# Kernel optimization log

Measured on AMD Instinct MI355X. Metric: run time of the kernel, lower is better.

## Reference

```python
import jax, jax.numpy as jnp
import numpy as np


def setup_inputs() -> dict:
    key = jax.random.key(0)
    k1, k2, k3 = jax.random.split(key, 3)
    B, H, S, D = 2, 16, 2048, 64
    q = jax.random.normal(k1, (B, H, S, D), dtype=jnp.float32)
    k = jax.random.normal(k2, (B, H, S, D), dtype=jnp.float32)
    v = jax.random.normal(k3, (B, H, S, D), dtype=jnp.float32)
    return {"q": q, "k": k, "v": v}


def reference(q, k, v):
    # q,k,v: [B,H,S,D]; causal attention with 1/sqrt(D) scaling, fp32 softmax.
    scale = 1.0 / (q.shape[-1] ** 0.5)
    scores = jnp.einsum('bhqd,bhkd->bhqk', q * scale, k)  # [B,H,S,S]
    S = scores.shape[-1]
    causal_mask = jnp.triu(jnp.ones((S, S), dtype=bool), k=1)
    scores = jnp.where(causal_mask, -jnp.inf, scores)
    attn = jax.nn.softmax(scores.astype(jnp.float32), axis=-1).astype(q.dtype)
    output = jnp.einsum('bhqk,bhkd->bhqd', attn, v)
    # Module also returns an all-zeros attn_weights placeholder of shape [B,H,S,S]
    attn_weights = jnp.zeros(scores.shape, dtype=q.dtype)
    return (output, attn_weights)
```

## Files before the change

kernel.cpp:

```cpp
#include <hip/hip_runtime.h>


typedef __bf16 bf16x8 __attribute__((ext_vector_type(8)));
typedef float f32x4 __attribute__((ext_vector_type(4)));

#define LOG2E 1.44269504088896340736f

__device__ __forceinline__ unsigned short f2bf(float f) {
  unsigned int u = __float_as_uint(f);
  u += 0x7fffu + ((u >> 16) & 1u);
  return (unsigned short)(u >> 16);
}

union U8 { unsigned short u[8]; bf16x8 v; };

constexpr int Sdim = 2048, Ddim = 64, BHn = 32;
constexpr int QTiles = Sdim / 64;
constexpr int LDK = 72;
constexpr int OUT0 = BHn * Sdim * Ddim;

__global__ __launch_bounds__(256, 2)
void flash_causal_kernel(const float* __restrict__ Q, const float* __restrict__ K,
                         const float* __restrict__ V, float* __restrict__ out) {
  __shared__ unsigned short Klds[64 * LDK];
  __shared__ unsigned short Vlds[Ddim * LDK];
  __shared__ unsigned short Plds[4][16 * LDK];

  const int tid  = threadIdx.x;
  const int wave = tid >> 6;
  const int lane = tid & 63;
  const int quad = lane >> 4;
  const int l15  = lane & 15;

  const int bh = blockIdx.x & (BHn - 1);
  const int g  = (int)(blockIdx.x >> 5);
  const int qt = (QTiles - 1) - g;

  const int base  = bh * Sdim * Ddim;
  const int qrow0 = qt * 64 + wave * 16;

  bf16x8 aq[2];
  {
    const float* qp = Q + base + (qrow0 + l15) * Ddim + quad * 8;
    #pragma unroll
    for (int s = 0; s < 2; ++s) {
      float4 a = *(const float4*)(qp + 32 * s);
      float4 b = *(const float4*)(qp + 32 * s + 4);
      U8 u;
      u.u[0] = f2bf(a.x * 0.125f); u.u[1] = f2bf(a.y * 0.125f);
      u.u[2] = f2bf(a.z * 0.125f); u.u[3] = f2bf(a.w * 0.125f);
      u.u[4] = f2bf(b.x * 0.125f); u.u[5] = f2bf(b.y * 0.125f);
      u.u[6] = f2bf(b.z * 0.125f); u.u[7] = f2bf(b.w * 0.125f);
      aq[s] = u.v;
    }
  }

  f32x4 ot[4];
  #pragma unroll
  for (int t = 0; t < 4; ++t) ot[t] = (f32x4){0.f, 0.f, 0.f, 0.f};
  float mrun = -__builtin_inff(), lrun = 0.f;

  const float4* kg4 = (const float4*)(K + base);
  const float4* vg4 = (const float4*)(V + base);

  float4 kf[4], vf[4];
  #pragma unroll
  for (int i = 0; i < 4; ++i) {
    kf[i] = kg4[i * 256 + tid];
    vf[i] = vg4[i * 256 + tid];
  }

  for (int j = 0; j <= qt; ++j) {
    __syncthreads();
    #pragma unroll
    for (int i = 0; i < 4; ++i) {
      int lin = i * 256 + tid;
      int row = lin >> 4;
      int c4  = (lin & 15) << 2;
      unsigned int k01 = (unsigned int)f2bf(kf[i].x) | ((unsigned int)f2bf(kf[i].y) << 16);
      unsigned int k23 = (unsigned int)f2bf(kf[i].z) | ((unsigned int)f2bf(kf[i].w) << 16);
      uint2 t2; t2.x = k01; t2.y = k23;
      *(uint2*)&Klds[row * LDK + c4] = t2;
      Vlds[(c4 + 0) * LDK + row] = f2bf(vf[i].x);
      Vlds[(c4 + 1) * LDK + row] = f2bf(vf[i].y);
      Vlds[(c4 + 2) * LDK + row] = f2bf(vf[i].z);
      Vlds[(c4 + 3) * LDK + row] = f2bf(vf[i].w);
    }
    __syncthreads();

    if (j < qt) {
      const float4* kp = kg4 + (j + 1) * 1024;
      const float4* vp = vg4 + (j + 1) * 1024;
      #pragma unroll
      for (int i = 0; i < 4; ++i) {
        kf[i] = kp[i * 256 + tid];
        vf[i] = vp[i * 256 + tid];
      }
    }

    f32x4 sc[4];
    #pragma unroll
    for (int t = 0; t < 4; ++t) sc[t] = (f32x4){0.f, 0.f, 0.f, 0.f};
    #pragma unroll
    for (int s = 0; s < 2; ++s) {
      #pragma unroll
      for (int t = 0; t < 4; ++t) {
        bf16x8 ka = *(const bf16x8*)&Klds[(16 * t + l15) * LDK + 32 * s + quad * 8];
        sc[t] = __builtin_amdgcn_mfma_f32_16x16x32_bf16(ka, aq[s], sc[t], 0, 0, 0);
      }
    }

    if (j == qt) {
      const int qml = wave * 16 + l15;
      #pragma unroll
      for (int t = 0; t < 4; ++t)
        #pragma unroll
        for (int r = 0; r < 4; ++r)
          if (16 * t + 4 * quad + r > qml) sc[t][r] = -__builtin_inff();
    }

    float mx = sc[0][0];
    #pragma unroll
    for (int t = 0; t < 4; ++t)
      #pragma unroll
      for (int r = 0; r < 4; ++r) mx = fmaxf(mx, sc[t][r]);
    mx = fmaxf(mx, __shfl_xor(mx, 16));
    mx = fmaxf(mx, __shfl_xor(mx, 32));
    float mn    = fmaxf(mrun, mx);
    float alpha = __builtin_amdgcn_exp2f((mrun - mn) * LOG2E);
    float msc   = mn * LOG2E;
    mrun = mn;
    float rs = 0.f;
    #pragma unroll
    for (int t = 0; t < 4; ++t)
      #pragma unroll
      for (int r = 0; r < 4; ++r) {
        float p = __builtin_amdgcn_exp2f(fmaf(sc[t][r], LOG2E, -msc));
        sc[t][r] = p;
        rs += p;
      }
    rs += __shfl_xor(rs, 16);
    rs += __shfl_xor(rs, 32);
    lrun = lrun * alpha + rs;
    #pragma unroll
    for (int t = 0; t < 4; ++t)
      #pragma unroll
      for (int r = 0; r < 4; ++r) ot[t][r] *= alpha;

    #pragma unroll
    for (int t = 0; t < 4; ++t) {
      uint2 pw;
      pw.x = (unsigned int)f2bf(sc[t][0]) | ((unsigned int)f2bf(sc[t][1]) << 16);
      pw.y = (unsigned int)f2bf(sc[t][2]) | ((unsigned int)f2bf(sc[t][3]) << 16);
      *(uint2*)&Plds[wave][l15 * LDK + 16 * t + 4 * quad] = pw;
    }

    #pragma unroll
    for (int s = 0; s < 2; ++s) {
      bf16x8 pb = *(const bf16x8*)&Plds[wave][l15 * LDK + 32 * s + quad * 8];
      #pragma unroll
      for (int t = 0; t < 4; ++t) {
        bf16x8 va = *(const bf16x8*)&Vlds[(16 * t + l15) * LDK + 32 * s + quad * 8];
        ot[t] = __builtin_amdgcn_mfma_f32_16x16x32_bf16(va, pb, ot[t], 0, 0, 0);
      }
    }
  }

  {
    float inv = 1.0f / lrun;
    float* orow = out + base + (qrow0 + l15) * Ddim + 4 * quad;
    #pragma unroll
    for (int t = 0; t < 4; ++t) {
      f32x4 o4;
      o4.x = ot[t][0] * inv; o4.y = ot[t][1] * inv;
      o4.z = ot[t][2] * inv; o4.w = ot[t][3] * inv;
      *(f32x4*)(orow + 16 * t) = o4;
    }
  }

  {
    const int w = 2 * g + 1;
    const size_t start_f4 = (size_t)1024 * (32 * (size_t)(g * g) + (size_t)bh * w);
    const size_t count_f4 = (size_t)1024 * w;
    f32x4 z4 = (f32x4){0.f, 0.f, 0.f, 0.f};
    f32x4* zp = (f32x4*)(out + OUT0) + start_f4;
    for (size_t i = tid; i < count_f4; i += 256)
      __builtin_nontemporal_store(z4, zp + i);
  }
}

extern "C" void kernel_launch(void* const* d_in, const int* in_sizes, int n_in,
                              void* d_out, int out_size, void* d_ws, size_t ws_size,
                              hipStream_t stream) {
  const float* q = (const float*)d_in[0];
  const float* k = (const float*)d_in[1];
  const float* v = (const float*)d_in[2];
  float* out = (float*)d_out;
  dim3 grid(BHn * QTiles);
  flash_causal_kernel<<<grid, dim3(256), 0, stream>>>(q, k, v, out);
}
```

Measured before the change: 621.1 us.

## Double-buffer K/V LDS tiles, swizzle V layout, interleave causal tile scheduling

K and V tiles now live in double-buffered LDS, so the next tile is staged while the current one is consumed, which drops one barrier per iteration. Global prefetch now runs two tiles ahead. The transposed V layout gets an XOR swizzle to reduce LDS bank conflicts on the scattered 16-bit writes and reads. Block-to-query-tile mapping alternates short and long causal rows to balance load, the occupancy hint rises from 2 to 3 blocks per CU, and the zero-fill indexing is remapped to match. In exchange, LDS use roughly doubles for K/V and register pressure grows, which may stop the higher occupancy from being reached.

```diff
diff --git a/kernel.cpp b/kernel.cpp
--- a/kernel.cpp
+++ b/kernel.cpp
@@ -12,18 +12,18 @@
   return (unsigned short)(u >> 16);
 }
 
-union U8 { unsigned short u[8]; bf16x8 v; };
-
 constexpr int Sdim = 2048, Ddim = 64, BHn = 32;
-constexpr int QTiles = Sdim / 64;
+constexpr int QTiles = 32;
 constexpr int LDK = 72;
 constexpr int OUT0 = BHn * Sdim * Ddim;
 
-__global__ __launch_bounds__(256, 2)
+__device__ __forceinline__ int vswz_m(int d) { return ((d >> 2) ^ (d >> 5)) & 7; }
+
+__global__ __launch_bounds__(256, 3)
 void flash_causal_kernel(const float* __restrict__ Q, const float* __restrict__ K,
                          const float* __restrict__ V, float* __restrict__ out) {
-  __shared__ unsigned short Klds[64 * LDK];
-  __shared__ unsigned short Vlds[Ddim * LDK];
+  __shared__ unsigned short Klds[2][64 * LDK];
+  __shared__ unsigned short Vlds[2][64 * LDK];
   __shared__ unsigned short Plds[4][16 * LDK];
 
   const int tid  = threadIdx.x;
@@ -34,7 +34,7 @@
 
   const int bh = blockIdx.x & (BHn - 1);
   const int g  = (int)(blockIdx.x >> 5);
-  const int qt = (QTiles - 1) - g;
+  const int qt = (g & 1) ? (QTiles - 1 - (g >> 1)) : (g >> 1);
 
   const int base  = bh * Sdim * Ddim;
   const int qrow0 = qt * 64 + wave * 16;
@@ -46,7 +46,7 @@
     for (int s = 0; s < 2; ++s) {
       float4 a = *(const float4*)(qp + 32 * s);
       float4 b = *(const float4*)(qp + 32 * s + 4);
-      U8 u;
+      union { unsigned short u[8]; bf16x8 v; } u;
       u.u[0] = f2bf(a.x * 0.125f); u.u[1] = f2bf(a.y * 0.125f);
       u.u[2] = f2bf(a.z * 0.125f); u.u[3] = f2bf(a.w * 0.125f);
       u.u[4] = f2bf(b.x * 0.125f); u.u[5] = f2bf(b.y * 0.125f);
@@ -64,39 +64,47 @@
   const float4* vg4 = (const float4*)(V + base);
 
   float4 kf[4], vf[4];
-  #pragma unroll
-  for (int i = 0; i < 4; ++i) {
-    kf[i] = kg4[i * 256 + tid];
-    vf[i] = vg4[i * 256 + tid];
-  }
-
-  for (int j = 0; j <= qt; ++j) {
-    __syncthreads();
+
+  auto stage = [&](int buf) {
     #pragma unroll
     for (int i = 0; i < 4; ++i) {
       int lin = i * 256 + tid;
       int row = lin >> 4;
       int c4  = (lin & 15) << 2;
-      unsigned int k01 = (unsigned int)f2bf(kf[i].x) | ((unsigned int)f2bf(kf[i].y) << 16);
-      unsigned int k23 = (unsigned int)f2bf(kf[i].z) | ((unsigned int)f2bf(kf[i].w) << 16);
-      uint2 t2; t2.x = k01; t2.y = k23;
-      *(uint2*)&Klds[row * LDK + c4] = t2;
-      Vlds[(c4 + 0) * LDK + row] = f2bf(vf[i].x);
-      Vlds[(c4 + 1) * LDK + row] = f2bf(vf[i].y);
-      Vlds[(c4 + 2) * LDK + row] = f2bf(vf[i].z);
-      Vlds[(c4 + 3) * LDK + row] = f2bf(vf[i].w);
-    }
+      uint2 t2;
+      t2.x = (unsigned int)f2bf(kf[i].x) | ((unsigned int)f2bf(kf[i].y) << 16);
+      t2.y = (unsigned int)f2bf(kf[i].z) | ((unsigned int)f2bf(kf[i].w) << 16);
+      *(uint2*)&Klds[buf][row * LDK + c4] = t2;
+      const int sw = vswz_m(c4) << 3;
+      Vlds[buf][(c4 + 0) * LDK + (row ^ sw)] = f2bf(vf[i].x);
+      Vlds[buf][(c4 + 1) * LDK + (row ^ sw)] = f2bf(vf[i].y);
+      Vlds[buf][(c4 + 2) * LDK + (row ^ sw)] = f2bf(vf[i].z);
+      Vlds[buf][(c4 + 3) * LDK + (row ^ sw)] = f2bf(vf[i].w);
+    }
+  };
+
+  #pragma unroll
+  for (int i = 0; i < 4; ++i) { kf[i] = kg4[i * 256 + tid]; vf[i] = vg4[i * 256 + tid]; }
+  stage(0);
+  if (qt >= 1) {
+    const float4* kp = kg4 + 1024;
+    const float4* vp = vg4 + 1024;
+    #pragma unroll
+    for (int i = 0; i < 4; ++i) { kf[i] = kp[i * 256 + tid]; vf[i] = vp[i * 256 + tid]; }
+  }
+
+  for (int j = 0; j <= qt; ++j) {
     __syncthreads();
-
-    if (j < qt) {
-      const float4* kp = kg4 + (j + 1) * 1024;
-      const float4* vp = vg4 + (j + 1) * 1024;
-      #pragma unroll
-      for (int i = 0; i < 4; ++i) {
-        kf[i] = kp[i * 256 + tid];
-        vf[i] = vp[i * 256 + tid];
-      }
-    }
+    if (j < qt) stage((j + 1) & 1);
+    if (j + 2 <= qt) {
+      const float4* kp = kg4 + (j + 2) * 1024;
+      const float4* vp = vg4 + (j + 2) * 1024;
+      #pragma unroll
+      for (int i = 0; i < 4; ++i) { kf[i] = kp[i * 256 + tid]; vf[i] = vp[i * 256 + tid]; }
+    }
+
+    const unsigned short* Kb = Klds[j & 1];
+    const unsigned short* Vb = Vlds[j & 1];
 
     f32x4 sc[4];
     #pragma unroll
@@ -105,7 +113,7 @@
     for (int s = 0; s < 2; ++s) {
       #pragma unroll
       for (int t = 0; t < 4; ++t) {
-        bf16x8 ka = *(const bf16x8*)&Klds[(16 * t + l15) * LDK + 32 * s + quad * 8];
+        bf16x8 ka = *(const bf16x8*)&Kb[(16 * t + l15) * LDK + 32 * s + quad * 8];
         sc[t] = __builtin_amdgcn_mfma_f32_16x16x32_bf16(ka, aq[s], sc[t], 0, 0, 0);
       }
     }
@@ -160,7 +168,9 @@
       bf16x8 pb = *(const bf16x8*)&Plds[wave][l15 * LDK + 32 * s + quad * 8];
       #pragma unroll
       for (int t = 0; t < 4; ++t) {
-        bf16x8 va = *(const bf16x8*)&Vlds[(16 * t + l15) * LDK + 32 * s + quad * 8];
+        const int d = 16 * t + l15;
+        const int knb = ((4 * s + quad) ^ vswz_m(d)) << 3;
+        bf16x8 va = *(const bf16x8*)&Vb[d * LDK + knb];
         ot[t] = __builtin_amdgcn_mfma_f32_16x16x32_bf16(va, pb, ot[t], 0, 0, 0);
       }
     }
@@ -179,8 +189,9 @@
   }
 
   {
-    const int w = 2 * g + 1;
-    const size_t start_f4 = (size_t)1024 * (32 * (size_t)(g * g) + (size_t)bh * w);
+    const int gp = (QTiles - 1) - qt;
+    const int w  = 2 * gp + 1;
+    const size_t start_f4 = (size_t)1024 * (32 * (size_t)(gp * gp) + (size_t)bh * w);
     const size_t count_f4 = (size_t)1024 * w;
     f32x4 z4 = (f32x4){0.f, 0.f, 0.f, 0.f};
     f32x4* zp = (f32x4*)(out + OUT0) + start_f4;
```

Result: faster. 598.1 us (-3.7%).
